# Kernel tuning notes

Measured on AMD Instinct MI355X. Metric: run time of the kernel, lower is better.

## Reference

```python
import jax, jax.numpy as jnp
import numpy as np

ALPHA = 0.2        # LeakyReLU negative slope
NEG_BIG = -9e15    # mask fill value from the original module


def setup_inputs() -> dict:
    key = jax.random.key(0)
    k1, k2, k3, k4 = jax.random.split(key, 4)
    B, N, F_in, F_out = 4, 4096, 128, 64
    h = jax.random.normal(k1, (B, N, F_in), dtype=jnp.float32)
    adj = jax.random.randint(k2, (N, N), 0, 2, dtype=jnp.int32)
    W = jax.random.normal(k3, (F_in, F_out), dtype=jnp.float32)
    a = jax.random.normal(k4, (2 * F_out, 1), dtype=jnp.float32)
    return {"h": h, "adj": adj, "W": W, "a": a}


def reference(h, adj, W, a):
    # h: [B, N, F_in], adj: [N, N], W: [F_in, F_out], a: [2*F_out, 1]
    F_out = W.shape[1]
    hW = jnp.einsum('bni,io->bno', h, W)               # [B, N, F_out]
    f1 = hW @ a[:F_out, :]                             # [B, N, 1]
    f2 = hW @ a[F_out:, :]                             # [B, N, 1]
    e = f1 + jnp.swapaxes(f2, 1, 2)                    # [B, N, N] broadcast-add
    e = jax.nn.leaky_relu(e, negative_slope=ALPHA)
    e = jax.nn.softmax(e, axis=2)
    # dropout is a no-op (is_training=False)
    attention = jnp.where(adj[None, :, :] > 0, e, NEG_BIG)
    new_h = jax.nn.sigmoid(jnp.einsum('bnm,bmo->bno', attention, hW))
    return new_h
```

## Files before the change

### kernel.cpp

```cpp
#include <hip/hip_runtime.h>
#include <hip/hip_bf16.h>


#define GN 4096
#define GB 4
#define FIN 128
#define FOUT 64

typedef int i32x4 __attribute__((ext_vector_type(4)));
typedef unsigned int uint32x4 __attribute__((ext_vector_type(4)));
typedef float f32x4 __attribute__((ext_vector_type(4)));

__global__ __launch_bounds__(256) void pack_kernel(const int* __restrict__ adj,
                                                   unsigned long long* __restrict__ tmask) {
    int wid = blockIdx.x * 4 + (threadIdx.x >> 6);
    int lane = threadIdx.x & 63;
    int rt = wid >> 6, s = wid & 63;
    int row16 = lane & 15, g = lane >> 4;
    const int* base = adj + (size_t)(rt * 64 + row16) * GN + s * 64 + g * 16;
    unsigned long long res = 0ull;
#pragma unroll
    for (int r = 0; r < 4; ++r) {
        const i32x4* p = (const i32x4*)(base + (size_t)r * 16 * GN);
        unsigned int b16 = 0;
#pragma unroll
        for (int q = 0; q < 4; ++q) {
            i32x4 v = p[q];
            b16 |= (v.x == 0 ? 1u : 0u) << (q * 4);
            b16 |= (v.y == 0 ? 2u : 0u) << (q * 4);
            b16 |= (v.z == 0 ? 4u : 0u) << (q * 4);
            b16 |= (v.w == 0 ? 8u : 0u) << (q * 4);
        }
        res |= (unsigned long long)b16 << (r * 16);
    }
    tmask[(size_t)wid * 64 + lane] = res;
}

__global__ __launch_bounds__(256) void hwrepack_kernel(const float* __restrict__ h,
                                                       const float* __restrict__ W,
                                                       double* __restrict__ hW,
                                                       unsigned char* __restrict__ Bp) {
    __shared__ float Wl[FIN][FOUT];
    const int t = threadIdx.x;
    const int o = t & 63, a = t >> 6;
    const int bx = (int)blockIdx.x;
    const int b = bx >> 8, rq = bx & 255;

    {
        const f32x4* Wv = (const f32x4*)W;
        f32x4* Wlv = (f32x4*)&Wl[0][0];
#pragma unroll
        for (int c = 0; c < 8; ++c)
            Wlv[c * 256 + t] = Wv[c * 256 + t];
    }
    __syncthreads();

    const int row0 = rq * 16 + a * 4;
    const float* h0 = h + ((size_t)b * GN + row0) * FIN;
    double ac0 = 0, ac1 = 0, ac2 = 0, ac3 = 0;
#pragma unroll 16
    for (int k = 0; k < FIN; ++k) {
        double wd = (double)Wl[k][o];
        ac0 = fma((double)h0[k],           wd, ac0);
        ac1 = fma((double)h0[k + FIN],     wd, ac1);
        ac2 = fma((double)h0[k + 2 * FIN], wd, ac2);
        ac3 = fma((double)h0[k + 3 * FIN], wd, ac3);
    }

    double* hwp = hW + ((size_t)b * GN + row0) * FOUT + o;
    hwp[0]       = ac0;
    hwp[FOUT]    = ac1;
    hwp[2 * FOUT] = ac2;
    hwp[3 * FOUT] = ac3;

    unsigned int w0 = 0, w1 = 0, w2 = 0;
    double accs[4] = {ac0, ac1, ac2, ac3};
#pragma unroll
    for (int rr = 0; rr < 4; ++rr) {
        int qi = (int)llrint(accs[rr] * 65536.0);
        int d0 = ((qi + 128) & 255) - 128; qi = (qi - d0) >> 8;
        int d1 = ((qi + 128) & 255) - 128; qi = (qi - d1) >> 8;
        w0 |= (unsigned int)(d0 & 255) << (rr * 8);
        w1 |= (unsigned int)(d1 & 255) << (rr * 8);
        w2 |= (unsigned int)(qi & 255) << (rr * 8);
    }
    const int q4 = rq * 4 + a;
    const int p = q4 >> 4, g = (q4 >> 2) & 3, qr = q4 & 3;
    const int cg = o >> 4, col16 = o & 15;
    unsigned char* dst = Bp + ((size_t)b * 64 + p) * 12288
                       + cg * 1024 + g * 256 + col16 * 16 + qr * 4;
    *(unsigned int*)(dst)        = w0;
    *(unsigned int*)(dst + 4096) = w1;
    *(unsigned int*)(dst + 8192) = w2;
}

__global__ __launch_bounds__(512, 1) void gemm_kernel(const unsigned char* __restrict__ Bp,
                                                      const unsigned long long* __restrict__ tmask,
                                                      const double* __restrict__ hW,
                                                      float* __restrict__ out) {
    __shared__ __align__(16) unsigned char lds[49152];
    __shared__ unsigned int nflag;
    __shared__ unsigned int flagbuf[128];
    __shared__ double fred[8];

    const int tid = threadIdx.x, lane = tid & 63, wv = tid >> 6;
    const int cg = wv & 3, kg = wv >> 2;
    const int rt = (int)blockIdx.x >> 2, b = (int)blockIdx.x & 3;
    if (tid == 0) nflag = 0;

    const unsigned char* bptr = Bp + (size_t)b * 786432 + kg * 12288 + cg * 1024 + lane * 16;
    const unsigned long long* mptr = tmask + (size_t)rt * 4096 + kg * 64 + lane;

    i32x4 acc[4][3];
#pragma unroll
    for (int r = 0; r < 4; ++r)
#pragma unroll
        for (int pl = 0; pl < 3; ++pl) {
            i32x4 z = {0, 0, 0, 0};
            acc[r][pl] = z;
        }

#define DECLSET(S) i32x4 b##S##0, b##S##1, b##S##2; unsigned long long m##S;
#define LOADSET(S, T) { const unsigned char* g_ = bptr + (size_t)(T) * 24576;          \
        b##S##0 = *(const i32x4*)(g_);                                                 \
        b##S##1 = *(const i32x4*)(g_ + 4096);                                          \
        b##S##2 = *(const i32x4*)(g_ + 8192);                                          \
        m##S = mptr[(size_t)(T) * 128]; }

    DECLSET(A) DECLSET(B) DECLSET(C) DECLSET(D)
    LOADSET(A, 0) LOADSET(B, 1) LOADSET(C, 2) LOADSET(D, 3)

    auto dostep = [&](unsigned long long mw, i32x4 v0, i32x4 v1, i32x4 v2) {
        const unsigned int mlo = (unsigned int)mw, mhi = (unsigned int)(mw >> 32);
#pragma unroll
        for (int r = 0; r < 4; ++r) {
            unsigned int half = (r >> 1) ? mhi : mlo;
            unsigned int w16 = (r & 1) ? (half >> 16) : (half & 0xFFFFu);
            uint32x4 u;
#pragma unroll
            for (int q = 0; q < 4; ++q)
                u[q] = (((w16 >> (4 * q)) & 0xFu) * 0x00204081u) & 0x01010101u;
            i32x4 af = __builtin_bit_cast(i32x4, u);
            acc[r][0] = __builtin_amdgcn_mfma_i32_16x16x64_i8(af, v0, acc[r][0], 0, 0, 0);
            acc[r][1] = __builtin_amdgcn_mfma_i32_16x16x64_i8(af, v1, acc[r][1], 0, 0, 0);
            acc[r][2] = __builtin_amdgcn_mfma_i32_16x16x64_i8(af, v2, acc[r][2], 0, 0, 0);
        }
    };

    for (int T = 0; T < 32; T += 4) {
        dostep(mA, bA0, bA1, bA2);
        if (T + 4 < 32) LOADSET(A, T + 4)
        dostep(mB, bB0, bB1, bB2);
        if (T + 5 < 32) LOADSET(B, T + 5)
        dostep(mC, bC0, bC1, bC2);
        if (T + 6 < 32) LOADSET(C, T + 6)
        dostep(mD, bD0, bD1, bD2);
        if (T + 7 < 32) LOADSET(D, T + 7)
    }
#undef DECLSET
#undef LOADSET

    __syncthreads();
    if (kg == 1) {
        unsigned char* dst = lds + cg * 12288 + lane * 192;
#pragma unroll
        for (int r = 0; r < 4; ++r)
#pragma unroll
            for (int pl = 0; pl < 3; ++pl)
                *(i32x4*)(dst + (r * 3 + pl) * 16) = acc[r][pl];
    }
    __syncthreads();
    if (kg == 0) {
        const unsigned char* s2 = lds + cg * 12288 + lane * 192;
#pragma unroll
        for (int r = 0; r < 4; ++r)
#pragma unroll
            for (int pl = 0; pl < 3; ++pl) {
                i32x4 v = *(const i32x4*)(s2 + (r * 3 + pl) * 16);
#pragma unroll
                for (int q = 0; q < 4; ++q) acc[r][pl][q] += v[q];
            }

        const int o = cg * 16 + (lane & 15);
#pragma unroll
        for (int r = 0; r < 4; ++r) {
#pragma unroll
            for (int q = 0; q < 4; ++q) {
                double S = (double)acc[r][0][q] + 256.0 * (double)acc[r][1][q]
                         + 65536.0 * (double)acc[r][2][q];
                int i = rt * 64 + r * 16 + (lane >> 4) * 4 + q;
                size_t oi = ((size_t)b * GN + i) * FOUT + o;
                out[oi] = S < 0.0 ? 1.0f : 0.0f;
                if (fabs(S) <= 2048.0) {
                    unsigned int idx = atomicAdd(&nflag, 1u);
                    if (idx < 128) flagbuf[idx] = ((unsigned int)i << 6) | (unsigned int)o;
                }
            }
        }
    }

    __syncthreads();
    unsigned int nf = nflag;
    if (nf > 128) nf = 128;
    for (unsigned int f = 0; f < nf; ++f) {
        unsigned int e = flagbuf[f];
        int o = e & 63;
        int i = (int)(e >> 6);
        int row16 = i & 15, r = (i >> 4) & 3;
        int s = tid >> 3, lg = (tid >> 1) & 3, hf = tid & 1;
        unsigned long long w = tmask[((size_t)rt * 64 + s) * 64 + (lg * 16 + row16)];
        double ps = 0.0;
        const double* hwc = hW + ((size_t)b * GN + s * 64 + lg * 16) * FOUT + o;
#pragma unroll
        for (int jj = hf * 8; jj < hf * 8 + 8; ++jj) {
            if ((w >> (r * 16 + jj)) & 1ull)
                ps += hwc[(size_t)jj * FOUT];
        }
#pragma unroll
        for (int d = 32; d >= 1; d >>= 1) ps += __shfl_down(ps, d, 64);
        if (lane == 0) fred[wv] = ps;
        __syncthreads();
        if (tid == 0) {
            double tot = ((fred[0] + fred[1]) + (fred[2] + fred[3]))
                       + ((fred[4] + fred[5]) + (fred[6] + fred[7]));
            out[((size_t)b * GN + i) * FOUT + o] = tot < 0.0 ? 1.0f : 0.0f;
        }
        __syncthreads();
    }
}

extern "C" void kernel_launch(void* const* d_in, const int* in_sizes, int n_in,
                              void* d_out, int out_size, void* d_ws, size_t ws_size,
                              hipStream_t stream) {
    const float* h   = (const float*)d_in[0];
    const int*   adj = (const int*)d_in[1];
    const float* W   = (const float*)d_in[2];
    float* out = (float*)d_out;

    char* ws = (char*)d_ws;
    double* hW                = (double*)ws;
    unsigned char* Bp         = (unsigned char*)(ws + 8388608);
    unsigned long long* tmask = (unsigned long long*)(ws + 12582912);

    pack_kernel<<<1024, 256, 0, stream>>>(adj, tmask);
    hwrepack_kernel<<<1024, 256, 0, stream>>>(h, W, hW, Bp);
    gemm_kernel<<<256, 512, 0, stream>>>(Bp, tmask, hW, out);
}
```

Measured before the change: 61.24 us.

## Coalesce adjacency packing via LDS transpose and stage h rows in LDS

The pack kernel now reads full contiguous 1024-column row segments of adj per warp, writes 16-bit masks to shared memory, then reassembles the tile-ordered 64-bit masks from LDS. This replaces the previous strided per-lane row access with coalesced loads. The hW kernel stages 32 rows of h in LDS with vector loads and gives each thread 8 output rows instead of 4, so each W element in LDS is reused more. Both launches use fewer, larger blocks, which means fewer waves in flight and more registers per thread.

```diff
diff --git a/kernel.cpp b/kernel.cpp
--- a/kernel.cpp
+++ b/kernel.cpp
@@ -13,27 +13,41 @@
 
 __global__ __launch_bounds__(256) void pack_kernel(const int* __restrict__ adj,
                                                    unsigned long long* __restrict__ tmask) {
-    int wid = blockIdx.x * 4 + (threadIdx.x >> 6);
-    int lane = threadIdx.x & 63;
-    int rt = wid >> 6, s = wid & 63;
-    int row16 = lane & 15, g = lane >> 4;
-    const int* base = adj + (size_t)(rt * 64 + row16) * GN + s * 64 + g * 16;
-    unsigned long long res = 0ull;
-#pragma unroll
-    for (int r = 0; r < 4; ++r) {
-        const i32x4* p = (const i32x4*)(base + (size_t)r * 16 * GN);
+    __shared__ unsigned short m16[64][68];
+    const int t = threadIdx.x;
+    const int rt = (int)blockIdx.x >> 2, cp = (int)blockIdx.x & 3;
+    const int wrow = t >> 6;
+    const int j16 = t & 63;
+
+#pragma unroll
+    for (int p = 0; p < 16; ++p) {
+        const int row = p * 4 + wrow;
+        const i32x4* src = (const i32x4*)(adj + (size_t)(rt * 64 + row) * GN
+                                          + cp * 1024 + j16 * 16);
         unsigned int b16 = 0;
 #pragma unroll
         for (int q = 0; q < 4; ++q) {
-            i32x4 v = p[q];
+            i32x4 v = src[q];
             b16 |= (v.x == 0 ? 1u : 0u) << (q * 4);
             b16 |= (v.y == 0 ? 2u : 0u) << (q * 4);
             b16 |= (v.z == 0 ? 4u : 0u) << (q * 4);
             b16 |= (v.w == 0 ? 8u : 0u) << (q * 4);
         }
-        res |= (unsigned long long)b16 << (r * 16);
-    }
-    tmask[(size_t)wid * 64 + lane] = res;
+        m16[row][j16] = (unsigned short)b16;
+    }
+    __syncthreads();
+
+#pragma unroll
+    for (int it = 0; it < 4; ++it) {
+        const int idx = it * 256 + t;
+        const int sloc = idx >> 6, l = idx & 63;
+        const int row16 = l & 15, g = l >> 4;
+        unsigned long long res = 0ull;
+#pragma unroll
+        for (int r = 0; r < 4; ++r)
+            res |= (unsigned long long)m16[r * 16 + row16][sloc * 4 + g] << (r * 16);
+        tmask[((size_t)rt * 64 + cp * 16 + sloc) * 64 + l] = res;
+    }
 }
 
 __global__ __launch_bounds__(256) void hwrepack_kernel(const float* __restrict__ h,
@@ -41,10 +55,11 @@
                                                        double* __restrict__ hW,
                                                        unsigned char* __restrict__ Bp) {
     __shared__ float Wl[FIN][FOUT];
+    __shared__ float hsf[32][FIN];
     const int t = threadIdx.x;
     const int o = t & 63, a = t >> 6;
     const int bx = (int)blockIdx.x;
-    const int b = bx >> 8, rq = bx & 255;
+    const int b = bx >> 7, rq = bx & 127;
 
     {
         const f32x4* Wv = (const f32x4*)W;
@@ -53,45 +68,61 @@
         for (int c = 0; c < 8; ++c)
             Wlv[c * 256 + t] = Wv[c * 256 + t];
     }
-    __syncthreads();
-
-    const int row0 = rq * 16 + a * 4;
-    const float* h0 = h + ((size_t)b * GN + row0) * FIN;
-    double ac0 = 0, ac1 = 0, ac2 = 0, ac3 = 0;
-#pragma unroll 16
-    for (int k = 0; k < FIN; ++k) {
-        double wd = (double)Wl[k][o];
-        ac0 = fma((double)h0[k],           wd, ac0);
-        ac1 = fma((double)h0[k + FIN],     wd, ac1);
-        ac2 = fma((double)h0[k + 2 * FIN], wd, ac2);
-        ac3 = fma((double)h0[k + 3 * FIN], wd, ac3);
+    {
+        const f32x4* src = (const f32x4*)(h + ((size_t)b * GN + rq * 32) * FIN);
+        f32x4* dst = (f32x4*)&hsf[0][0];
+#pragma unroll
+        for (int c = 0; c < 4; ++c)
+            dst[c * 256 + t] = src[c * 256 + t];
+    }
+    __syncthreads();
+
+    const int row0 = rq * 32 + a * 8;
+    double ac[8];
+#pragma unroll
+    for (int rr = 0; rr < 8; ++rr) ac[rr] = 0.0;
+
+#pragma unroll
+    for (int k4 = 0; k4 < 32; ++k4) {
+        f32x4 hv[8];
+#pragma unroll
+        for (int rr = 0; rr < 8; ++rr)
+            hv[rr] = *(const f32x4*)&hsf[a * 8 + rr][k4 * 4];
+#pragma unroll
+        for (int j = 0; j < 4; ++j) {
+            double wd = (double)Wl[k4 * 4 + j][o];
+#pragma unroll
+            for (int rr = 0; rr < 8; ++rr)
+                ac[rr] = fma((double)hv[rr][j], wd, ac[rr]);
+        }
     }
 
     double* hwp = hW + ((size_t)b * GN + row0) * FOUT + o;
-    hwp[0]       = ac0;
-    hwp[FOUT]    = ac1;
-    hwp[2 * FOUT] = ac2;
-    hwp[3 * FOUT] = ac3;
-
-    unsigned int w0 = 0, w1 = 0, w2 = 0;
-    double accs[4] = {ac0, ac1, ac2, ac3};
-#pragma unroll
-    for (int rr = 0; rr < 4; ++rr) {
-        int qi = (int)llrint(accs[rr] * 65536.0);
-        int d0 = ((qi + 128) & 255) - 128; qi = (qi - d0) >> 8;
-        int d1 = ((qi + 128) & 255) - 128; qi = (qi - d1) >> 8;
-        w0 |= (unsigned int)(d0 & 255) << (rr * 8);
-        w1 |= (unsigned int)(d1 & 255) << (rr * 8);
-        w2 |= (unsigned int)(qi & 255) << (rr * 8);
-    }
-    const int q4 = rq * 4 + a;
-    const int p = q4 >> 4, g = (q4 >> 2) & 3, qr = q4 & 3;
-    const int cg = o >> 4, col16 = o & 15;
-    unsigned char* dst = Bp + ((size_t)b * 64 + p) * 12288
-                       + cg * 1024 + g * 256 + col16 * 16 + qr * 4;
-    *(unsigned int*)(dst)        = w0;
-    *(unsigned int*)(dst + 4096) = w1;
-    *(unsigned int*)(dst + 8192) = w2;
+#pragma unroll
+    for (int rr = 0; rr < 8; ++rr)
+        hwp[(size_t)rr * FOUT] = ac[rr];
+
+#pragma unroll
+    for (int u = 0; u < 2; ++u) {
+        unsigned int w0 = 0, w1 = 0, w2 = 0;
+#pragma unroll
+        for (int rr = 0; rr < 4; ++rr) {
+            int qi = (int)llrint(ac[u * 4 + rr] * 65536.0);
+            int d0 = ((qi + 128) & 255) - 128; qi = (qi - d0) >> 8;
+            int d1 = ((qi + 128) & 255) - 128; qi = (qi - d1) >> 8;
+            w0 |= (unsigned int)(d0 & 255) << (rr * 8);
+            w1 |= (unsigned int)(d1 & 255) << (rr * 8);
+            w2 |= (unsigned int)(qi & 255) << (rr * 8);
+        }
+        const int q4 = (row0 >> 2) + u;
+        const int p = q4 >> 4, g = (q4 >> 2) & 3, qr = q4 & 3;
+        const int cg = o >> 4, col16 = o & 15;
+        unsigned char* dst = Bp + ((size_t)b * 64 + p) * 12288
+                           + cg * 1024 + g * 256 + col16 * 16 + qr * 4;
+        *(unsigned int*)(dst)        = w0;
+        *(unsigned int*)(dst + 4096) = w1;
+        *(unsigned int*)(dst + 8192) = w2;
+    }
 }
 
 __global__ __launch_bounds__(512, 1) void gemm_kernel(const unsigned char* __restrict__ Bp,
@@ -242,7 +273,7 @@
     unsigned char* Bp         = (unsigned char*)(ws + 8388608);
     unsigned long long* tmask = (unsigned long long*)(ws + 12582912);
 
-    pack_kernel<<<1024, 256, 0, stream>>>(adj, tmask);
-    hwrepack_kernel<<<1024, 256, 0, stream>>>(h, W, hW, Bp);
+    pack_kernel<<<256, 256, 0, stream>>>(adj, tmask);
+    hwrepack_kernel<<<512, 256, 0, stream>>>(h, W, hW, Bp);
     gemm_kernel<<<256, 512, 0, stream>>>(Bp, tmask, hW, out);
 }
```

Measured after the change: 55.62 us. 9.2% less time.
